# Kernel optimization log

Hardware: AMD Instinct MI355X
Metric: run time of the kernel (lower is better)

Reference implementation:

```python
import jax, jax.numpy as jnp
import numpy as np

DIMS = 4

def mlp(x, W1, b1, W2, b2, W3, b3, Wo, bo):
    # x: (4,) -> scalar log(g_rr)
    h = jnp.tanh(x @ W1 + b1)
    h = jnp.tanh(h @ W2 + b2)
    h = jnp.tanh(h @ W3 + b3)
    return (h @ Wo + bo)[0]

def metric(x, params):
    # build_g: spherical metric with learned g_rr = exp(net(x))
    g_rr = jnp.exp(mlp(x, *params))
    r, th = x[1], x[2]
    diag = jnp.stack([-jnp.ones(()), g_rr, r ** 2, (r * jnp.sin(th)) ** 2])
    return jnp.diag(diag)  # (4,4)

def christoffel(x, params):
    g = metric(x, params)
    dg = jax.jacfwd(lambda xx: metric(xx, params))(x)  # dg[i,j,k] = d g_ij / d x^k
    g_inv = jnp.linalg.inv(g)
    # Gamma^a_bc = 0.5 g^{ad} (d_c g_db + d_b g_dc - d_d g_bc)
    sym = dg + jnp.transpose(dg, (0, 2, 1)) - jnp.transpose(dg, (2, 0, 1))
    gamma = 0.5 * jnp.einsum('ad,dbc->abc', g_inv, sym)
    return gamma, g_inv

def einstein_per_sample(x, params):
    gamma, g_inv = christoffel(x, params)
    # D[a,i,j,k] = d_k Gamma^a_ij (second nested forward-mode jacobian)
    D = jax.jacfwd(lambda xx: christoffel(xx, params)[0])(x)
    # R^a_bcd = d_c Gamma^a_db - d_d Gamma^a_cb + G^a_ce G^e_db - G^a_de G^e_cb
    riemann = (jnp.einsum('adbc->abcd', D) - jnp.einsum('acbd->abcd', D)
               + jnp.einsum('ace,edb->abcd', gamma, gamma)
               - jnp.einsum('ade,ecb->abcd', gamma, gamma))
    ricci = jnp.einsum('abad->bd', riemann)
    ricci_scalar = jnp.einsum('bd,bd->', g_inv, ricci)
    ricci_up = jnp.einsum('ac,bd,cd->ab', g_inv, g_inv, ricci)
    return ricci_up - 0.5 * g_inv * ricci_scalar  # contravariant Einstein tensor


def setup_inputs() -> dict:
    key = jax.random.key(0)
    ks = jax.random.split(key, 5)
    B, H = 8192, 256
    # coords in a well-conditioned region (avoid r ~ 0 which makes g singular)
    coords = jax.random.uniform(ks[0], (B, DIMS), dtype=jnp.float32) * 0.9 + 0.1
    def w(k, shape):
        fan_in = shape[0]
        return jax.random.normal(k, shape, dtype=jnp.float32) / np.sqrt(fan_in)
    return {
        'coords': coords,
        'W1': w(ks[1], (DIMS, H)), 'b1': jnp.zeros((H,), jnp.float32),
        'W2': w(ks[2], (H, H)),   'b2': jnp.zeros((H,), jnp.float32),
        'W3': w(ks[3], (H, H)),   'b3': jnp.zeros((H,), jnp.float32),
        'Wo': w(ks[4], (H, 1)),   'bo': jnp.zeros((1,), jnp.float32),
    }


def reference(coords, W1, b1, W2, b2, W3, b3, Wo, bo):
    params = (W1, b1, W2, b2, W3, b3, Wo, bo)
    # Batched Einstein tensor G^{ab}(x) for every sample: (B, 4, 4)
    return jax.vmap(lambda x: einstein_per_sample(x, params))(coords)
```

## Files before the change

### kernel.cpp

```cpp
#include <hip/hip_runtime.h>
#include <math.h>

typedef _Float16 half8 __attribute__((ext_vector_type(8)));
typedef float floatx4 __attribute__((ext_vector_type(4)));

#define HDIM 256
#define NC 15
#define NCP 16
#define SPB 8
#define MR 128
#define NWAVE 4
#define NT 4


__device__ __forceinline__ float ftanh(float x) {
    float e = __expf(2.f * x);
    return fmaf(-2.f, __builtin_amdgcn_rcpf(e + 1.f), 1.f);
}

__device__ __forceinline__ void einstein_tail(
    float f, const float* Gf, const float* Hs, float r, float th,
    float* __restrict__ outp)
{
    float Hf[4][4];
    {
        int qq = 0;
#pragma unroll
        for (int k = 0; k < 4; ++k)
#pragma unroll
            for (int l = k; l < 4; ++l) { Hf[k][l] = Hs[qq]; Hf[l][k] = Hs[qq]; ++qq; }
    }
    float sn = sinf(th), cs = cosf(th);
    float E  = expf(f);

    float gd[4] = {-1.f, E, r * r, r * r * sn * sn};
    float gi[4];
#pragma unroll
    for (int a = 0; a < 4; ++a) gi[a] = 1.f / gd[a];

    float dgv[4][4];
    float ddg[4][4][4];
#pragma unroll
    for (int a = 0; a < 4; ++a)
#pragma unroll
        for (int k = 0; k < 4; ++k) {
            dgv[a][k] = 0.f;
#pragma unroll
            for (int l = 0; l < 4; ++l) ddg[a][k][l] = 0.f;
        }
#pragma unroll
    for (int k = 0; k < 4; ++k) dgv[1][k] = E * Gf[k];
    dgv[2][1] = 2.f * r;
    dgv[3][1] = 2.f * r * sn * sn;
    dgv[3][2] = 2.f * r * r * sn * cs;
#pragma unroll
    for (int k = 0; k < 4; ++k)
#pragma unroll
        for (int l = 0; l < 4; ++l)
            ddg[1][k][l] = E * fmaf(Gf[k], Gf[l], Hf[k][l]);
    ddg[2][1][1] = 2.f;
    ddg[3][1][1] = 2.f * sn * sn;
    ddg[3][1][2] = 4.f * r * sn * cs;
    ddg[3][2][1] = 4.f * r * sn * cs;
    ddg[3][2][2] = 2.f * r * r * (cs * cs - sn * sn);

    auto SYMF = [&](int a, int i, int jx) -> float {
        float sy = 0.f;
        if (a == i)  sy += dgv[a][jx];
        if (a == jx) sy += dgv[a][i];
        if (i == jx) sy -= dgv[i][a];
        return sy;
    };
    auto DF = [&](int a, int i, int jx, int k) -> float {
        float ds = 0.f;
        if (a == i)  ds += ddg[a][jx][k];
        if (a == jx) ds += ddg[a][i][k];
        if (i == jx) ds -= ddg[i][a][k];
        return 0.5f * (gi[a] * ds - gi[a] * gi[a] * dgv[a][k] * SYMF(a, i, jx));
    };

    float Gm[4][4][4];
#pragma unroll
    for (int a = 0; a < 4; ++a)
#pragma unroll
        for (int i = 0; i < 4; ++i)
#pragma unroll
            for (int jx = 0; jx < 4; ++jx)
                Gm[a][i][jx] = 0.5f * gi[a] * SYMF(a, i, jx);

    float ric[4][4];
#pragma unroll
    for (int b = 0; b < 4; ++b)
#pragma unroll
        for (int d = 0; d < 4; ++d) {
            float sum = 0.f;
#pragma unroll
            for (int a = 0; a < 4; ++a) {
                sum += DF(a, d, b, a) - DF(a, a, b, d);
#pragma unroll
                for (int e = 0; e < 4; ++e)
                    sum += Gm[a][a][e] * Gm[e][d][b] - Gm[a][d][e] * Gm[e][a][b];
            }
            ric[b][d] = sum;
        }

    float Rs = 0.f;
#pragma unroll
    for (int b = 0; b < 4; ++b) Rs += gi[b] * ric[b][b];

#pragma unroll
    for (int a = 0; a < 4; ++a)
#pragma unroll
        for (int b = 0; b < 4; ++b) {
            float v = gi[a] * gi[b] * ric[a][b];
            if (a == b) v -= 0.5f * gi[a] * Rs;
            outp[a * 4 + b] = v;
        }
}

__global__ __launch_bounds__(64) void einstein_k(
    const float* __restrict__ coords, const float* __restrict__ bo,
    float* io, int B)
{
    const int s = blockIdx.x * 64 + threadIdx.x;
    if (s >= B) return;
    float4 f0 = *(const float4*)&io[s * 16 + 0];
    float4 f1 = *(const float4*)&io[s * 16 + 4];
    float4 f2 = *(const float4*)&io[s * 16 + 8];
    float4 f3 = *(const float4*)&io[s * 16 + 12];
    float f = f0.x + bo[0];
    float Gf[4] = {f0.y, f0.z, f0.w, f1.x};
    float Hs[10] = {f1.y, f1.z, f1.w, f2.x, f2.y, f2.z, f2.w, f3.x, f3.y, f3.z};
    float r  = coords[s * 4 + 1];
    float th = coords[s * 4 + 2];
    float res[16];
    einstein_tail(f, Gf, Hs, r, th, res);
#pragma unroll
    for (int e = 0; e < 4; ++e)
        *(float4*)&io[s * 16 + e * 4] =
            make_float4(res[e*4+0], res[e*4+1], res[e*4+2], res[e*4+3]);
}

__global__ __launch_bounds__(256) void pack_wt(
    const float* __restrict__ W2, const float* __restrict__ W3,
    _Float16* __restrict__ Wt)
{
    __shared__ float t[64][65];
    const int m    = blockIdx.x >> 4;
    const float* W = m ? W3 : W2;
    const int tile = blockIdx.x & 15;
    const int k0 = (tile >> 2) * 64, j0 = (tile & 3) * 64;
    const int tx = threadIdx.x & 63, ty = threadIdx.x >> 6;
#pragma unroll
    for (int i = 0; i < 16; ++i) {
        int k = ty + i * 4;
        t[k][tx] = W[(k0 + k) * HDIM + j0 + tx];
    }
    __syncthreads();
#pragma unroll
    for (int i = 0; i < 16; ++i) {
        int jj = ty + i * 4;
        Wt[(size_t)m * HDIM * HDIM + (j0 + jj) * HDIM + k0 + tx] =
            (_Float16)t[tx][jj];
    }
}

template <bool TW>
__global__ __launch_bounds__(256, 2) void mlp_fused(
    const float* __restrict__ coords,
    const float* __restrict__ W1, const float* __restrict__ b1,
    const float* __restrict__ W2, const float* __restrict__ b2,
    const float* __restrict__ W3, const float* __restrict__ b3,
    const float* __restrict__ Wo,
    const _Float16* __restrict__ Wt,
    float* __restrict__ out, int B)
{
    __shared__ __align__(16) _Float16 st[MR * HDIM];

    const int tid  = threadIdx.x;
    const int w    = tid >> 6;
    const int lane = tid & 63;
    const int col  = lane & 15;
    const int q    = lane >> 4;
    const int s0   = blockIdx.x * SPB;

    floatx4 acc[8][NT];

    auto f4get = [](const float4& v, int i) -> float {
        switch (i & 3) { case 0: return v.x; case 1: return v.y;
                         case 2: return v.z; default: return v.w; }
    };

    auto produce1 = [&]() {
        const int sl = tid & 7;
        const int tc = tid >> 3;
        int ss = s0 + sl; if (ss >= B) ss = B - 1;
        const float x0 = coords[ss * 4 + 0];
        const float x1 = coords[ss * 4 + 1];
        const float x2 = coords[ss * 4 + 2];
        const float x3 = coords[ss * 4 + 3];
        const int jg = tc * 8;
        float4 wa[4][2];
#pragma unroll
        for (int k = 0; k < 4; ++k) {
            wa[k][0] = *(const float4*)&W1[k * HDIM + jg];
            wa[k][1] = *(const float4*)&W1[k * HDIM + jg + 4];
        }
        float4 bb0 = *(const float4*)&b1[jg];
        float4 bb1 = *(const float4*)&b1[jg + 4];
        half8 ch[NCP];
#pragma unroll
        for (int jj = 0; jj < 8; ++jj) ch[15][jj] = (_Float16)0.f;
#pragma unroll
        for (int jj = 0; jj < 8; ++jj) {
            const int h = jj >> 2;
            float w0 = f4get(wa[0][h], jj), w1 = f4get(wa[1][h], jj);
            float w2v = f4get(wa[2][h], jj), w3v = f4get(wa[3][h], jj);
            float a = f4get(h ? bb1 : bb0, jj);
            a = fmaf(x0, w0, a); a = fmaf(x1, w1, a);
            a = fmaf(x2, w2v, a); a = fmaf(x3, w3v, a);
            float v = ftanh(a), tp = 1.f - v * v, m2 = -2.f * v * tp;
            float g[4] = {w0, w1, w2v, w3v};
            ch[0][jj] = (_Float16)v;
#pragma unroll
            for (int k = 0; k < 4; ++k) ch[1 + k][jj] = (_Float16)(tp * g[k]);
            int idx = 5;
#pragma unroll
            for (int aa = 0; aa < 4; ++aa)
#pragma unroll
                for (int bb2 = aa; bb2 < 4; ++bb2) {
                    ch[idx][jj] = (_Float16)(m2 * g[aa] * g[bb2]); ++idx;
                }
        }
#pragma unroll
        for (int c = 0; c < NCP; ++c) {
            const int m = 16 * (c >> 1) + 4 * (sl >> 1) + 2 * (sl & 1) + (c & 1);
            const int addr = m * HDIM + (((tc ^ m) & 31) << 3);
            *(half8*)&st[addr] = ch[c];
        }
    };

    auto init_acc = [&](const float* __restrict__ b) {
#pragma unroll
        for (int nt = 0; nt < NT; ++nt) {
            float bj = b[w * 64 + nt * 16 + col];
#pragma unroll
            for (int mt = 0; mt < 8; ++mt)
#pragma unroll
                for (int r = 0; r < 4; ++r) acc[mt][nt][r] = 0.f;
            acc[0][nt][0] = bj;
            acc[0][nt][2] = bj;
        }
    };

    auto gemm_full = [&](const float* __restrict__ W, int layer) {
        half8 bf[2][NT];
#pragma unroll
        for (int nt = 0; nt < NT; ++nt) {
            const int j = w * 64 + nt * 16 + col;
            if constexpr (TW) {
                bf[0][nt] = *(const half8*)&Wt[((size_t)layer * HDIM + j) * HDIM + q * 8];
            } else {
#pragma unroll
                for (int i = 0; i < 8; ++i)
                    bf[0][nt][i] = (_Float16)W[(q * 8 + i) * HDIM + j];
            }
        }
#pragma unroll
        for (int ks = 0; ks < 8; ++ks) {
            const int cur = ks & 1, nxt = cur ^ 1;
            if (ks < 7) {
                const int kg2 = (ks + 1) * 32 + q * 8;
#pragma unroll
                for (int nt = 0; nt < NT; ++nt) {
                    const int j = w * 64 + nt * 16 + col;
                    if constexpr (TW) {
                        bf[nxt][nt] = *(const half8*)&Wt[((size_t)layer * HDIM + j) * HDIM + kg2];
                    } else {
#pragma unroll
                        for (int i = 0; i < 8; ++i)
                            bf[nxt][nt][i] = (_Float16)W[(kg2 + i) * HDIM + j];
                    }
                }
            }
            const int lc = ks * 4 + q;
            half8 af[8];
#pragma unroll
            for (int mt = 0; mt < 8; ++mt) {
                const int m = 16 * mt + col;
                af[mt] = *(const half8*)&st[m * HDIM + (((lc ^ m) & 31) << 3)];
            }
#pragma unroll
            for (int mt = 0; mt < 8; ++mt)
#pragma unroll
                for (int nt = 0; nt < NT; ++nt)
                    acc[mt][nt] = __builtin_amdgcn_mfma_f32_16x16x32_f16(
                        af[mt], bf[cur][nt], acc[mt][nt], 0, 0, 0);
        }
    };

    auto transform_store = [&]() {
#pragma unroll
        for (int nt = 0; nt < NT; ++nt) {
            const int j = w * 64 + nt * 16 + col;
            const int jc = j >> 3, jb = j & 7;
#pragma unroll
            for (int sv = 0; sv < 2; ++sv) {
                float pre[NCP];
#pragma unroll
                for (int c = 0; c < NCP; ++c)
                    pre[c] = acc[c >> 1][nt][sv * 2 + (c & 1)];
                float v = ftanh(pre[0]), tp = 1.f - v * v, m2 = -2.f * v * tp;
                float g[4] = {pre[1], pre[2], pre[3], pre[4]};
                float ns[NCP];
                ns[0] = v;
#pragma unroll
                for (int k = 0; k < 4; ++k) ns[1 + k] = tp * g[k];
                int idx = 5;
#pragma unroll
                for (int aa = 0; aa < 4; ++aa)
#pragma unroll
                    for (int bb2 = aa; bb2 < 4; ++bb2) {
                        ns[idx] = fmaf(tp, pre[idx], m2 * g[aa] * g[bb2]); ++idx;
                    }
                ns[15] = 0.f;
#pragma unroll
                for (int c = 0; c < NCP; ++c) {
                    const int m = 16 * (c >> 1) + 4 * q + 2 * sv + (c & 1);
                    st[m * HDIM + (((jc ^ m) & 31) << 3) + jb] = (_Float16)ns[c];
                }
            }
        }
    };

    produce1();
    __syncthreads();
    init_acc(b2);
    gemm_full(W2, 0);
    __syncthreads();
    transform_store();
    __syncthreads();
    init_acc(b3);
    gemm_full(W3, 1);

    __syncthreads();
    float* part = (float*)st;
    float wo[NT];
#pragma unroll
    for (int nt = 0; nt < NT; ++nt) wo[nt] = Wo[w * 64 + nt * 16 + col];

    float on2[2][NC];
#pragma unroll
    for (int sv = 0; sv < 2; ++sv)
#pragma unroll
        for (int c = 0; c < NC; ++c) on2[sv][c] = 0.f;
#pragma unroll
    for (int nt = 0; nt < NT; ++nt)
#pragma unroll
        for (int sv = 0; sv < 2; ++sv) {
            float pre[NCP];
#pragma unroll
            for (int c = 0; c < NCP; ++c)
                pre[c] = acc[c >> 1][nt][sv * 2 + (c & 1)];
            float v = ftanh(pre[0]), tp = 1.f - v * v, m2 = -2.f * v * tp;
            float g[4] = {pre[1], pre[2], pre[3], pre[4]};
            on2[sv][0] = fmaf(wo[nt], v, on2[sv][0]);
#pragma unroll
            for (int k = 0; k < 4; ++k)
                on2[sv][1 + k] = fmaf(wo[nt], tp * g[k], on2[sv][1 + k]);
            int idx = 5;
#pragma unroll
            for (int aa = 0; aa < 4; ++aa)
#pragma unroll
                for (int bb2 = aa; bb2 < 4; ++bb2) {
                    on2[sv][idx] = fmaf(wo[nt],
                        fmaf(tp, pre[idx], m2 * g[aa] * g[bb2]), on2[sv][idx]);
                    ++idx;
                }
        }
#pragma unroll
    for (int mask = 1; mask < 16; mask <<= 1)
#pragma unroll
        for (int sv = 0; sv < 2; ++sv)
#pragma unroll
            for (int c = 0; c < NC; ++c)
                on2[sv][c] += __shfl_xor(on2[sv][c], mask, 64);
    if (col == 0) {
#pragma unroll
        for (int sv = 0; sv < 2; ++sv)
#pragma unroll
            for (int c = 0; c < NC; ++c)
                part[(w * SPB + 2 * q + sv) * NC + c] = on2[sv][c];
    }
    __syncthreads();
    if (tid < SPB * NC) {
        const int sl = tid / NC, c = tid % NC;
        float v = 0.f;
#pragma unroll
        for (int ww = 0; ww < NWAVE; ++ww) v += part[(ww * SPB + sl) * NC + c];
        int s = s0 + sl;
        if (s < B) out[s * 16 + c] = v;
    }
}

extern "C" void kernel_launch(void* const* d_in, const int* in_sizes, int n_in,
                              void* d_out, int out_size, void* d_ws, size_t ws_size,
                              hipStream_t stream) {
    const float* coords = (const float*)d_in[0];
    const float* W1 = (const float*)d_in[1];
    const float* b1 = (const float*)d_in[2];
    const float* W2 = (const float*)d_in[3];
    const float* b2 = (const float*)d_in[4];
    const float* W3 = (const float*)d_in[5];
    const float* b3 = (const float*)d_in[6];
    const float* Wo = (const float*)d_in[7];
    const float* bo = (const float*)d_in[8];
    float* out = (float*)d_out;
    const int B = in_sizes[0] / 4;
    const int nblocks = (B + SPB - 1) / SPB;

    const size_t wt_bytes = (size_t)2 * HDIM * HDIM * sizeof(_Float16);
    if (ws_size >= wt_bytes) {
        _Float16* Wt = (_Float16*)d_ws;
        pack_wt<<<32, 256, 0, stream>>>(W2, W3, Wt);
        mlp_fused<true><<<nblocks, 256, 0, stream>>>(
            coords, W1, b1, W2, b2, W3, b3, Wo, Wt, out, B);
    } else {
        mlp_fused<false><<<nblocks, 256, 0, stream>>>(
            coords, W1, b1, W2, b2, W3, b3, Wo, nullptr, out, B);
    }
    einstein_k<<<(B + 63) / 64, 64, 0, stream>>>(coords, bo, out, B);
}
```

Before: 124.3 us.

## Run two staggered wave teams per block to overlap MLP stages

Each block now has 512 threads split into two 256-thread teams, each with its own LDS tile and its own 8 samples. The teams are offset by one stage, so one team's transform/tanh/epilogue work runs while the other team's MFMA GEMM runs. The intent is to overlap VALU and LDS phases with matrix-core phases inside a workgroup. In exchange, LDS per block doubles to 128 KB and launch bounds rise to 512 threads, which may lower occupancy or add register pressure. The added barriers also force the two teams into lockstep.

```diff
diff --git a/kernel.cpp b/kernel.cpp
--- a/kernel.cpp
+++ b/kernel.cpp
@@ -166,7 +166,7 @@
 }
 
 template <bool TW>
-__global__ __launch_bounds__(256, 2) void mlp_fused(
+__global__ __launch_bounds__(512, 2) void mlp_fused(
     const float* __restrict__ coords,
     const float* __restrict__ W1, const float* __restrict__ b1,
     const float* __restrict__ W2, const float* __restrict__ b2,
@@ -175,14 +175,19 @@
     const _Float16* __restrict__ Wt,
     float* __restrict__ out, int B)
 {
-    __shared__ __align__(16) _Float16 st[MR * HDIM];
+    __shared__ __align__(16) _Float16 st[2][MR * HDIM];
 
     const int tid  = threadIdx.x;
-    const int w    = tid >> 6;
+    const int team = tid >> 8;
+    const int ttid = tid & 255;
+    const int w    = ttid >> 6;
     const int lane = tid & 63;
     const int col  = lane & 15;
     const int q    = lane >> 4;
-    const int s0   = blockIdx.x * SPB;
+    const int s0   = blockIdx.x * (2 * SPB);
+    const int sb   = s0 + team * SPB;
+
+    _Float16* __restrict__ stT = st[team];
 
     floatx4 acc[8][NT];
 
@@ -192,9 +197,9 @@
     };
 
     auto produce1 = [&]() {
-        const int sl = tid & 7;
-        const int tc = tid >> 3;
-        int ss = s0 + sl; if (ss >= B) ss = B - 1;
+        const int sl = ttid & 7;
+        const int tc = ttid >> 3;
+        int ss = sb + sl; if (ss >= B) ss = B - 1;
         const float x0 = coords[ss * 4 + 0];
         const float x1 = coords[ss * 4 + 1];
         const float x2 = coords[ss * 4 + 2];
@@ -236,7 +241,7 @@
         for (int c = 0; c < NCP; ++c) {
             const int m = 16 * (c >> 1) + 4 * (sl >> 1) + 2 * (sl & 1) + (c & 1);
             const int addr = m * HDIM + (((tc ^ m) & 31) << 3);
-            *(half8*)&st[addr] = ch[c];
+            *(half8*)&stT[addr] = ch[c];
         }
     };
 
@@ -288,7 +293,7 @@
 #pragma unroll
             for (int mt = 0; mt < 8; ++mt) {
                 const int m = 16 * mt + col;
-                af[mt] = *(const half8*)&st[m * HDIM + (((lc ^ m) & 31) << 3)];
+                af[mt] = *(const half8*)&stT[m * HDIM + (((lc ^ m) & 31) << 3)];
             }
 #pragma unroll
             for (int mt = 0; mt < 8; ++mt)
@@ -327,80 +332,94 @@
 #pragma unroll
                 for (int c = 0; c < NCP; ++c) {
                     const int m = 16 * (c >> 1) + 4 * q + 2 * sv + (c & 1);
-                    st[m * HDIM + (((jc ^ m) & 31) << 3) + jb] = (_Float16)ns[c];
+                    stT[m * HDIM + (((jc ^ m) & 31) << 3) + jb] = (_Float16)ns[c];
                 }
             }
         }
     };
 
-    produce1();
-    __syncthreads();
-    init_acc(b2);
-    gemm_full(W2, 0);
-    __syncthreads();
-    transform_store();
-    __syncthreads();
-    init_acc(b3);
-    gemm_full(W3, 1);
-
-    __syncthreads();
-    float* part = (float*)st;
-    float wo[NT];
-#pragma unroll
-    for (int nt = 0; nt < NT; ++nt) wo[nt] = Wo[w * 64 + nt * 16 + col];
-
-    float on2[2][NC];
-#pragma unroll
-    for (int sv = 0; sv < 2; ++sv)
-#pragma unroll
-        for (int c = 0; c < NC; ++c) on2[sv][c] = 0.f;
-#pragma unroll
-    for (int nt = 0; nt < NT; ++nt)
-#pragma unroll
-        for (int sv = 0; sv < 2; ++sv) {
-            float pre[NCP];
-#pragma unroll
-            for (int c = 0; c < NCP; ++c)
-                pre[c] = acc[c >> 1][nt][sv * 2 + (c & 1)];
-            float v = ftanh(pre[0]), tp = 1.f - v * v, m2 = -2.f * v * tp;
-            float g[4] = {pre[1], pre[2], pre[3], pre[4]};
-            on2[sv][0] = fmaf(wo[nt], v, on2[sv][0]);
-#pragma unroll
-            for (int k = 0; k < 4; ++k)
-                on2[sv][1 + k] = fmaf(wo[nt], tp * g[k], on2[sv][1 + k]);
-            int idx = 5;
-#pragma unroll
-            for (int aa = 0; aa < 4; ++aa)
-#pragma unroll
-                for (int bb2 = aa; bb2 < 4; ++bb2) {
-                    on2[sv][idx] = fmaf(wo[nt],
-                        fmaf(tp, pre[idx], m2 * g[aa] * g[bb2]), on2[sv][idx]);
-                    ++idx;
-                }
-        }
-#pragma unroll
-    for (int mask = 1; mask < 16; mask <<= 1)
+    auto epilogue_part = [&]() {
+        float* part = (float*)stT;
+        float wo[NT];
+#pragma unroll
+        for (int nt = 0; nt < NT; ++nt) wo[nt] = Wo[w * 64 + nt * 16 + col];
+
+        float on2[2][NC];
 #pragma unroll
         for (int sv = 0; sv < 2; ++sv)
 #pragma unroll
-            for (int c = 0; c < NC; ++c)
-                on2[sv][c] += __shfl_xor(on2[sv][c], mask, 64);
-    if (col == 0) {
-#pragma unroll
-        for (int sv = 0; sv < 2; ++sv)
-#pragma unroll
-            for (int c = 0; c < NC; ++c)
-                part[(w * SPB + 2 * q + sv) * NC + c] = on2[sv][c];
-    }
-    __syncthreads();
-    if (tid < SPB * NC) {
-        const int sl = tid / NC, c = tid % NC;
-        float v = 0.f;
-#pragma unroll
-        for (int ww = 0; ww < NWAVE; ++ww) v += part[(ww * SPB + sl) * NC + c];
-        int s = s0 + sl;
-        if (s < B) out[s * 16 + c] = v;
-    }
+            for (int c = 0; c < NC; ++c) on2[sv][c] = 0.f;
+#pragma unroll
+        for (int nt = 0; nt < NT; ++nt)
+#pragma unroll
+            for (int sv = 0; sv < 2; ++sv) {
+                float pre[NCP];
+#pragma unroll
+                for (int c = 0; c < NCP; ++c)
+                    pre[c] = acc[c >> 1][nt][sv * 2 + (c & 1)];
+                float v = ftanh(pre[0]), tp = 1.f - v * v, m2 = -2.f * v * tp;
+                float g[4] = {pre[1], pre[2], pre[3], pre[4]};
+                on2[sv][0] = fmaf(wo[nt], v, on2[sv][0]);
+#pragma unroll
+                for (int k = 0; k < 4; ++k)
+                    on2[sv][1 + k] = fmaf(wo[nt], tp * g[k], on2[sv][1 + k]);
+                int idx = 5;
+#pragma unroll
+                for (int aa = 0; aa < 4; ++aa)
+#pragma unroll
+                    for (int bb2 = aa; bb2 < 4; ++bb2) {
+                        on2[sv][idx] = fmaf(wo[nt],
+                            fmaf(tp, pre[idx], m2 * g[aa] * g[bb2]), on2[sv][idx]);
+                        ++idx;
+                    }
+            }
+#pragma unroll
+        for (int mask = 1; mask < 16; mask <<= 1)
+#pragma unroll
+            for (int sv = 0; sv < 2; ++sv)
+#pragma unroll
+                for (int c = 0; c < NC; ++c)
+                    on2[sv][c] += __shfl_xor(on2[sv][c], mask, 64);
+        if (col == 0) {
+#pragma unroll
+            for (int sv = 0; sv < 2; ++sv)
+#pragma unroll
+                for (int c = 0; c < NC; ++c)
+                    part[(w * SPB + 2 * q + sv) * NC + c] = on2[sv][c];
+        }
+    };
+
+    auto final_reduce = [&]() {
+        float* part = (float*)stT;
+        if (ttid < SPB * NC) {
+            const int sl = ttid / NC, c = ttid % NC;
+            float v = 0.f;
+#pragma unroll
+            for (int ww = 0; ww < NWAVE; ++ww)
+                v += part[(ww * SPB + sl) * NC + c];
+            int s = sb + sl;
+            if (s < B) out[s * 16 + c] = v;
+        }
+    };
+
+    if (team == 0) produce1();
+    __syncthreads();
+    if (team == 0) { init_acc(b2); gemm_full(W2, 0); }
+    else produce1();
+    __syncthreads();
+    if (team == 0) transform_store();
+    else { init_acc(b2); gemm_full(W2, 0); }
+    __syncthreads();
+    if (team == 0) { init_acc(b3); gemm_full(W3, 1); }
+    else transform_store();
+    __syncthreads();
+    if (team == 0) epilogue_part();
+    else { init_acc(b3); gemm_full(W3, 1); }
+    __syncthreads();
+    if (team == 0) final_reduce();
+    else epilogue_part();
+    __syncthreads();
+    if (team == 1) final_reduce();
 }
 
 extern "C" void kernel_launch(void* const* d_in, const int* in_sizes, int n_in,
@@ -417,16 +436,16 @@
     const float* bo = (const float*)d_in[8];
     float* out = (float*)d_out;
     const int B = in_sizes[0] / 4;
-    const int nblocks = (B + SPB - 1) / SPB;
+    const int nblocks = (B + 2 * SPB - 1) / (2 * SPB);
 
     const size_t wt_bytes = (size_t)2 * HDIM * HDIM * sizeof(_Float16);
     if (ws_size >= wt_bytes) {
         _Float16* Wt = (_Float16*)d_ws;
         pack_wt<<<32, 256, 0, stream>>>(W2, W3, Wt);
-        mlp_fused<true><<<nblocks, 256, 0, stream>>>(
+        mlp_fused<true><<<nblocks, 512, 0, stream>>>(
             coords, W1, b1, W2, b2, W3, b3, Wo, Wt, out, B);
     } else {
-        mlp_fused<false><<<nblocks, 256, 0, stream>>>(
+        mlp_fused<false><<<nblocks, 512, 0, stream>>>(
             coords, W1, b1, W2, b2, W3, b3, Wo, nullptr, out, B);
     }
     einstein_k<<<(B + 63) / 64, 64, 0, stream>>>(coords, bo, out, B);
```

After: 119.8 us. 1.04x faster.
